# Performance work log

Measured on AMD Instinct MI355X. Metric: run time of the kernel, lower is better.

The kernel has to match this reference:

```python
import jax, jax.numpy as jnp
import numpy as np

DIM = 1024
HEADS = 16
HEAD_DIM = DIM // HEADS
MLP_HID = 4 * DIM
EPS = 1e-5


def layer_norm(x, g, b):
    mu = jnp.mean(x, axis=-1, keepdims=True)
    var = jnp.mean(jnp.square(x - mu), axis=-1, keepdims=True)
    return (x - mu) * jax.lax.rsqrt(var + EPS) * g + b


def setup_inputs() -> dict:
    key = jax.random.key(0)
    ks = jax.random.split(key, 8)
    s_in = 1.0 / np.sqrt(DIM)
    s_hid = 1.0 / np.sqrt(MLP_HID)
    return {
        "x": jax.random.normal(ks[0], (4, 2048, DIM), dtype=jnp.float32),
        "qkv_w": jax.random.uniform(ks[1], (3 * DIM, DIM), jnp.float32, -s_in, s_in),
        "proj_w": jax.random.uniform(ks[2], (DIM, DIM), jnp.float32, -s_in, s_in),
        "proj_b": jnp.zeros((DIM,), jnp.float32),
        "ln1_g": jnp.ones((DIM,), jnp.float32),
        "ln1_b": jnp.zeros((DIM,), jnp.float32),
        "w1": jax.random.uniform(ks[3], (MLP_HID, DIM), jnp.float32, -s_in, s_in),
        "b1": jnp.zeros((MLP_HID,), jnp.float32),
        "prelu_a": jnp.asarray(0.25, jnp.float32),
        "w2": jax.random.uniform(ks[4], (DIM, MLP_HID), jnp.float32, -s_hid, s_hid),
        "b2": jnp.zeros((DIM,), jnp.float32),
        "ln2_g": jnp.ones((DIM,), jnp.float32),
        "ln2_b": jnp.zeros((DIM,), jnp.float32),
    }


def reference(x, qkv_w, proj_w, proj_b, ln1_g, ln1_b, w1, b1, prelu_a, w2, b2, ln2_g, ln2_b):
    B, N, C = x.shape
    scale = HEAD_DIM ** (-0.5)

    # Multi-head self-attention (full NxN scores, softmax over keys)
    qkv = (x @ qkv_w.T).reshape(B, N, 3, HEADS, HEAD_DIM)
    qkv = jnp.transpose(qkv, (2, 0, 3, 1, 4))  # [3, B, H, N, hd]
    q, k, v = qkv[0] * scale, qkv[1], qkv[2]
    attn = jax.nn.softmax(jnp.einsum("bhnd,bhmd->bhnm", q, k), axis=-1)
    o = jnp.einsum("bhnm,bhmd->bhnd", attn, v)
    o = jnp.transpose(o, (0, 2, 1, 3)).reshape(B, N, C)
    o = o @ proj_w.T + proj_b

    # Post-norm residual 1
    x = layer_norm(x + o, ln1_g, ln1_b)

    # MLP: Linear -> (Dropout=identity in eval) -> PReLU -> Linear
    h = x @ w1.T + b1
    h = jnp.where(h >= 0, h, prelu_a * h)
    h = h @ w2.T + b2

    # Post-norm residual 2
    return layer_norm(x + h, ln2_g, ln2_b)
```

## Files before the change

kernel.cpp:

```cpp
#include <hip/hip_runtime.h>


typedef __attribute__((ext_vector_type(8))) short short8;
typedef __attribute__((ext_vector_type(4))) short short4v;
typedef __attribute__((ext_vector_type(4))) float floatx4;
typedef __attribute__((ext_vector_type(4))) int int4v;

__device__ __forceinline__ float bf2f(unsigned short u) {
    return __uint_as_float(((unsigned int)u) << 16);
}
__device__ __forceinline__ unsigned short f2bf(float f) {
    unsigned int u = __float_as_uint(f);
    u += 0x7FFFu + ((u >> 16) & 1u);
    return (unsigned short)(u >> 16);
}
__device__ __forceinline__ int pack2bf(float a, float b) {
    return (int)f2bf(a) | ((int)f2bf(b) << 16);
}
__device__ __forceinline__ unsigned int cvt_pk_bf16(float lo, float hi) {
    unsigned int r;
    asm("v_cvt_pk_bf16_f32 %0, %1, %2" : "=v"(r) : "v"(lo), "v"(hi));
    return r;
}

#define Q_PRESCALE 0.18033688011112043f

#if __has_builtin(__builtin_amdgcn_exp2f)
__device__ __forceinline__ float fast_exp2(float x) { return __builtin_amdgcn_exp2f(x); }
#else
__device__ __forceinline__ float fast_exp2(float x) { return __expf(x * 0.6931471805599453f); }
#endif

#if __has_builtin(__builtin_amdgcn_permlane32_swap) && __has_builtin(__builtin_amdgcn_permlane16_swap)
#define HAVE_PERMLANE 1
#else
#define HAVE_PERMLANE 0
#endif

__device__ __forceinline__ void async16(const unsigned short* g, unsigned short* l) {
    __builtin_amdgcn_global_load_lds(
        (const __attribute__((address_space(1))) unsigned int*)g,
        (__attribute__((address_space(3))) unsigned int*)l, 16, 0, 0);
}

__global__ __launch_bounds__(256)
void cvt_f2b(const float* __restrict__ in, unsigned short* __restrict__ out) {
    const int i = (blockIdx.x * 256 + threadIdx.x) * 4;
    float4 v = *(const float4*)&in[i];
    short4v o;
    o[0] = (short)f2bf(v.x); o[1] = (short)f2bf(v.y);
    o[2] = (short)f2bf(v.z); o[3] = (short)f2bf(v.w);
    *(short4v*)&out[i] = o;
}

__global__ __launch_bounds__(256)
void gemm_bt(const unsigned short* __restrict__ A,
             const unsigned short* __restrict__ W,
             const float* __restrict__ bias,
             const float* __restrict__ prelu,
             unsigned short* __restrict__ C,
             int N, int K, int qcols) {
    __shared__ alignas(16) unsigned short lA[128 * 64];
    __shared__ alignas(16) unsigned short lB[128 * 64];

    const int m0 = blockIdx.x * 128;
    const int n0 = blockIdx.y * 128;
    const int tid  = threadIdx.x;
    const int lane = tid & 63;
    const int wave = tid >> 6;
    const int wm = (wave >> 1) * 64;
    const int wn = (wave & 1) * 64;
    const int lr = lane & 15;
    const int lq = lane >> 4;

    floatx4 acc[4][4] = {};

    for (int k0 = 0; k0 < K; k0 += 64) {
        #pragma unroll
        for (int it = 0; it < 4; ++it) {
            const int i = it * 256 + tid;
            const int row = i >> 3;
            const int col = (i & 7) << 3;
            unsigned short* dstA = &lA[(it * 256 + wave * 64) * 8];
            unsigned short* dstB = &lB[(it * 256 + wave * 64) * 8];
            async16(&A[(size_t)(m0 + row) * K + k0 + col], dstA);
            async16(&W[(size_t)(n0 + row) * K + k0 + col], dstB);
        }
        __syncthreads();
        #pragma unroll
        for (int s = 0; s < 2; ++s) {
            short8 af[4], bfr[4];
            #pragma unroll
            for (int i = 0; i < 4; ++i)
                af[i] = *(const short8*)&lA[(wm + i * 16 + lr) * 64 + s * 32 + lq * 8];
            #pragma unroll
            for (int j = 0; j < 4; ++j)
                bfr[j] = *(const short8*)&lB[(wn + j * 16 + lr) * 64 + s * 32 + lq * 8];
            #pragma unroll
            for (int i = 0; i < 4; ++i)
                #pragma unroll
                for (int j = 0; j < 4; ++j)
                    acc[i][j] = __builtin_amdgcn_mfma_f32_16x16x32_bf16(
                        af[i], bfr[j], acc[i][j], 0, 0, 0);
        }
        __syncthreads();
    }

    const bool has_prelu = (prelu != nullptr);
    const float slope = has_prelu ? prelu[0] : 0.f;
    #pragma unroll
    for (int j = 0; j < 4; ++j) {
        int gc = n0 + wn + j * 16 + lr;
        float bv = bias ? bias[gc] : 0.f;
        const float cscale = (gc < qcols) ? Q_PRESCALE : 1.f;
        #pragma unroll
        for (int i = 0; i < 4; ++i) {
            int gr = m0 + wm + i * 16 + lq * 4;
            #pragma unroll
            for (int r = 0; r < 4; ++r) {
                float v = acc[i][j][r] + bv;
                if (has_prelu && v < 0.f) v *= slope;
                C[(size_t)(gr + r) * N + gc] = f2bf(v * cscale);
            }
        }
    }
}

__global__ __launch_bounds__(256)
void transpose_v(const unsigned short* __restrict__ qkv,
                 unsigned short* __restrict__ vt) {
    const int kt = blockIdx.x;
    const int bh = blockIdx.y;
    const int b = bh >> 4, h = bh & 15;
    __shared__ unsigned short tile[64 * 65];
    for (int t = threadIdx.x; t < 512; t += 256) {
        const int key = t >> 3, c8 = (t & 7) << 3;
        short8 v8 = *(const short8*)&qkv[((size_t)(b * 2048 + kt * 64 + key)) * 3072 +
                                         2048 + h * 64 + c8];
        #pragma unroll
        for (int e = 0; e < 8; ++e)
            tile[key * 65 + c8 + e] = (unsigned short)v8[e];
    }
    __syncthreads();
    for (int t = threadIdx.x; t < 512; t += 256) {
        const int d = t >> 3, k8 = (t & 7) << 3;
        short8 o;
        #pragma unroll
        for (int e = 0; e < 8; ++e)
            o[e] = (short)tile[(k8 + e) * 65 + d];
        *(short8*)&vt[((size_t)bh * 64 + d) * 2048 + kt * 64 + k8] = o;
    }
}

__global__ __launch_bounds__(256, 2)
void attn_kernel(const unsigned short* __restrict__ qkv,
                 const unsigned short* __restrict__ vt,
                 unsigned short* __restrict__ o_attn) {
    const int id = blockIdx.x;
    const int qg = id >> 6;
    const int bh = id & 63;
    const int b = bh >> 4, h = bh & 15;
    const int tid  = threadIdx.x;
    const int lane = tid & 63;
    const int wave = tid >> 6;
    const int lr = lane & 15;
    const int lq = lane >> 4;
    const int q0 = (qg * 4 + wave) * 64;
    const size_t row0 = (size_t)(b * 2048) * 3072;

    __shared__ alignas(16) unsigned short lK[2][64 * 64];
    __shared__ alignas(16) unsigned short lV[2][64 * 64];

    short8 qf[4][2];
    #pragma unroll
    for (int j = 0; j < 4; ++j)
        #pragma unroll
        for (int s = 0; s < 2; ++s)
            qf[j][s] = *(const short8*)&qkv[row0 + (size_t)(q0 + j * 16 + lr) * 3072 +
                                            h * 64 + s * 32 + lq * 8];

    floatx4 oacc[4][4] = {};
    float l_i[4] = {0.f, 0.f, 0.f, 0.f};

    const int srow = lane >> 3;
    const int scol = (((lane & 7) ^ srow)) << 3;
    const int kx = lr & 7;

    auto stage = [&](int bi, int kc) {
        #pragma unroll
        for (int it2 = 0; it2 < 2; ++it2) {
            const int it = wave * 2 + it2;
            const int row = it * 8 + srow;
            async16(&qkv[row0 + (size_t)(kc + row) * 3072 + 1024 + h * 64 + scol],
                    &lK[bi][it * 512 + lane * 8]);
            async16(&vt[((size_t)bh * 64 + row) * 2048 + kc + scol],
                    &lV[bi][it * 512 + lane * 8]);
        }
    };

    asm volatile("s_waitcnt vmcnt(0)" ::: "memory");
    stage(0, 0);

    #pragma unroll 1
    for (int c = 0; c < 32; ++c) {
        const int cur = c & 1;
        if (c + 1 < 32) {
            stage(cur ^ 1, (c + 1) * 64);
            asm volatile("s_waitcnt vmcnt(4)" ::: "memory");
        } else {
            asm volatile("s_waitcnt vmcnt(0)" ::: "memory");
        }
        __builtin_amdgcn_s_barrier();
        asm volatile("" ::: "memory");

        floatx4 sacc[4][4] = {};
        #pragma unroll
        for (int s = 0; s < 2; ++s) {
            short8 kf[4];
            #pragma unroll
            for (int i = 0; i < 4; ++i) {
                const int r = i * 16 + lr;
                kf[i] = *(const short8*)&lK[cur][r * 64 + (((s * 4 + lq) ^ kx) << 3)];
            }
            #pragma unroll
            for (int i = 0; i < 4; ++i)
                #pragma unroll
                for (int j = 0; j < 4; ++j)
                    sacc[i][j] = __builtin_amdgcn_mfma_f32_16x16x32_bf16(
                        kf[i], qf[j][s], sacc[i][j], 0, 0, 0);
        }

        unsigned int pkd[4][4][2];
        #pragma unroll
        for (int i = 0; i < 4; ++i)
            #pragma unroll
            for (int j = 0; j < 4; ++j) {
                const float e0 = fast_exp2(sacc[i][j][0]);
                const float e1 = fast_exp2(sacc[i][j][1]);
                const float e2 = fast_exp2(sacc[i][j][2]);
                const float e3 = fast_exp2(sacc[i][j][3]);
                l_i[j] += (e0 + e1) + (e2 + e3);
                pkd[i][j][0] = cvt_pk_bf16(e0, e1);
                pkd[i][j][1] = cvt_pk_bf16(e2, e3);
            }

        #pragma unroll
        for (int s = 0; s < 2; ++s) {
            short8 vf[4];
            #pragma unroll
            for (int i = 0; i < 4; ++i) {
                const int r = i * 16 + lr;
                vf[i] = *(const short8*)&lV[cur][r * 64 + (((s * 4 + lq) ^ kx) << 3)];
            }
            short8 bq[4];
            #pragma unroll
            for (int j = 0; j < 4; ++j) {
                int4v iv;
#if HAVE_PERMLANE
                auto p0 = __builtin_amdgcn_permlane32_swap(
                    pkd[2 * s][j][0], pkd[2 * s + 1][j][0], false, false);
                auto w0 = __builtin_amdgcn_permlane16_swap(p0[0], p0[1], false, false);
                auto p1 = __builtin_amdgcn_permlane32_swap(
                    pkd[2 * s][j][1], pkd[2 * s + 1][j][1], false, false);
                auto w1 = __builtin_amdgcn_permlane16_swap(p1[0], p1[1], false, false);
                iv[0] = (int)w0[0]; iv[1] = (int)w1[0];
                iv[2] = (int)w0[1]; iv[3] = (int)w1[1];
#else
                const int src0 = lr + ((lq & 1) * 2) * 16;
                const int src1 = src0 + 16;
                const bool hi = (lq >> 1) != 0;
                int a0 = __shfl((int)pkd[2 * s][j][0], src0, 64);
                int c0 = __shfl((int)pkd[2 * s + 1][j][0], src0, 64);
                int a1 = __shfl((int)pkd[2 * s][j][1], src0, 64);
                int c1 = __shfl((int)pkd[2 * s + 1][j][1], src0, 64);
                int a2 = __shfl((int)pkd[2 * s][j][0], src1, 64);
                int c2 = __shfl((int)pkd[2 * s + 1][j][0], src1, 64);
                int a3 = __shfl((int)pkd[2 * s][j][1], src1, 64);
                int c3 = __shfl((int)pkd[2 * s + 1][j][1], src1, 64);
                iv[0] = hi ? c0 : a0;
                iv[1] = hi ? c1 : a1;
                iv[2] = hi ? c2 : a2;
                iv[3] = hi ? c3 : a3;
#endif
                bq[j] = __builtin_bit_cast(short8, iv);
            }
            #pragma unroll
            for (int j = 0; j < 4; ++j)
                #pragma unroll
                for (int i = 0; i < 4; ++i)
                    oacc[i][j] = __builtin_amdgcn_mfma_f32_16x16x32_bf16(
                        vf[i], bq[j], oacc[i][j], 0, 0, 0);
        }

        asm volatile("s_waitcnt lgkmcnt(0)" ::: "memory");
        __builtin_amdgcn_s_barrier();
        asm volatile("" ::: "memory");
    }

    #pragma unroll
    for (int j = 0; j < 4; ++j) {
        l_i[j] += __shfl_xor(l_i[j], 16, 64);
        l_i[j] += __shfl_xor(l_i[j], 32, 64);
        const float rl = 1.f / l_i[j];
        const int q = q0 + j * 16 + lr;
        #pragma unroll
        for (int i = 0; i < 4; ++i) {
            int2 pk;
            pk.x = pack2bf(oacc[i][j][0] * rl, oacc[i][j][1] * rl);
            pk.y = pack2bf(oacc[i][j][2] * rl, oacc[i][j][3] * rl);
            *(int2*)&o_attn[((size_t)(b * 2048 + q)) * 1024 + h * 64 + i * 16 + lq * 4] = pk;
        }
    }
}

__global__ __launch_bounds__(256)
void ln_f32_bf16(const float* __restrict__ x,
                 const unsigned short* __restrict__ res,
                 const float* __restrict__ g,
                 const float* __restrict__ bta,
                 unsigned short* __restrict__ out) {
    const int row = blockIdx.x;
    const int t = threadIdx.x;
    const size_t base = (size_t)row * 1024;

    float4 xv = *(const float4*)&x[base + t * 4];
    short4v rv = *(const short4v*)&res[base + t * 4];
    float v[4] = { xv.x + bf2f((unsigned short)rv[0]),
                   xv.y + bf2f((unsigned short)rv[1]),
                   xv.z + bf2f((unsigned short)rv[2]),
                   xv.w + bf2f((unsigned short)rv[3]) };
    float s = 0.f, s2 = 0.f;
    #pragma unroll
    for (int k = 0; k < 4; ++k) { s += v[k]; s2 += v[k] * v[k]; }
    #pragma unroll
    for (int off = 32; off > 0; off >>= 1) {
        s  += __shfl_xor(s, off, 64);
        s2 += __shfl_xor(s2, off, 64);
    }
    __shared__ float red[8];
    const int wave = t >> 6;
    if ((t & 63) == 0) { red[wave] = s; red[4 + wave] = s2; }
    __syncthreads();
    s  = red[0] + red[1] + red[2] + red[3];
    s2 = red[4] + red[5] + red[6] + red[7];
    const float mean = s * (1.f / 1024.f);
    const float var  = fmaxf(s2 * (1.f / 1024.f) - mean * mean, 0.f);
    const float inv  = rsqrtf(var + 1e-5f);

    short4v ov;
    #pragma unroll
    for (int k = 0; k < 4; ++k) {
        int c = t * 4 + k;
        ov[k] = (short)f2bf((v[k] - mean) * inv * g[c] + bta[c]);
    }
    *(short4v*)&out[base + t * 4] = ov;
}

__global__ __launch_bounds__(256)
void ln_bf16_f32(const unsigned short* __restrict__ x,
                 const unsigned short* __restrict__ res,
                 const float* __restrict__ g,
                 const float* __restrict__ bta,
                 float* __restrict__ out) {
    const int row = blockIdx.x;
    const int t = threadIdx.x;
    const size_t base = (size_t)row * 1024;

    short4v xv = *(const short4v*)&x[base + t * 4];
    short4v rv = *(const short4v*)&res[base + t * 4];
    float v[4];
    float s = 0.f, s2 = 0.f;
    #pragma unroll
    for (int k = 0; k < 4; ++k) {
        v[k] = bf2f((unsigned short)xv[k]) + bf2f((unsigned short)rv[k]);
        s += v[k];
        s2 += v[k] * v[k];
    }
    #pragma unroll
    for (int off = 32; off > 0; off >>= 1) {
        s  += __shfl_xor(s, off, 64);
        s2 += __shfl_xor(s2, off, 64);
    }
    __shared__ float red[8];
    const int wave = t >> 6;
    if ((t & 63) == 0) { red[wave] = s; red[4 + wave] = s2; }
    __syncthreads();
    s  = red[0] + red[1] + red[2] + red[3];
    s2 = red[4] + red[5] + red[6] + red[7];
    const float mean = s * (1.f / 1024.f);
    const float var  = fmaxf(s2 * (1.f / 1024.f) - mean * mean, 0.f);
    const float inv  = rsqrtf(var + 1e-5f);

    float4 ov;
    ov.x = (v[0] - mean) * inv * g[t * 4 + 0] + bta[t * 4 + 0];
    ov.y = (v[1] - mean) * inv * g[t * 4 + 1] + bta[t * 4 + 1];
    ov.z = (v[2] - mean) * inv * g[t * 4 + 2] + bta[t * 4 + 2];
    ov.w = (v[3] - mean) * inv * g[t * 4 + 3] + bta[t * 4 + 3];
    *(float4*)&out[base + t * 4] = ov;
}

extern "C" void kernel_launch(void* const* d_in, const int* in_sizes, int n_in,
                              void* d_out, int out_size, void* d_ws, size_t ws_size,
                              hipStream_t stream) {
    const float* x      = (const float*)d_in[0];
    const float* qkv_w  = (const float*)d_in[1];
    const float* proj_w = (const float*)d_in[2];
    const float* proj_b = (const float*)d_in[3];
    const float* ln1_g  = (const float*)d_in[4];
    const float* ln1_b  = (const float*)d_in[5];
    const float* w1     = (const float*)d_in[6];
    const float* b1     = (const float*)d_in[7];
    const float* prelu  = (const float*)d_in[8];
    const float* w2     = (const float*)d_in[9];
    const float* b2     = (const float*)d_in[10];
    const float* ln2_g  = (const float*)d_in[11];
    const float* ln2_b  = (const float*)d_in[12];
    float* out = (float*)d_out;

    char* ws = (char*)d_ws;
    const size_t MB = 1024 * 1024;
    unsigned short* wqkvb  = (unsigned short*)(ws);
    unsigned short* wprojb = (unsigned short*)(ws + 6 * MB);
    unsigned short* w1b    = (unsigned short*)(ws + 8 * MB);
    unsigned short* w2b    = (unsigned short*)(ws + 16 * MB);
    unsigned short* xb     = (unsigned short*)(ws + 24 * MB);
    unsigned short* vtb    = (unsigned short*)(ws + 24 * MB);
    unsigned short* qkvb   = (unsigned short*)(ws + 40 * MB);
    unsigned short* oat    = (unsigned short*)(ws + 88 * MB);
    unsigned short* pout   = (unsigned short*)(ws + 24 * MB);
    unsigned short* x1b    = (unsigned short*)(ws + 40 * MB);
    unsigned short* h1     = (unsigned short*)(ws + 56 * MB);
    unsigned short* h2     = (unsigned short*)(ws + 24 * MB);

    cvt_f2b<<<8192, 256, 0, stream>>>(x,      xb);
    cvt_f2b<<<3072, 256, 0, stream>>>(qkv_w,  wqkvb);
    cvt_f2b<<<1024, 256, 0, stream>>>(proj_w, wprojb);
    cvt_f2b<<<4096, 256, 0, stream>>>(w1,     w1b);
    cvt_f2b<<<4096, 256, 0, stream>>>(w2,     w2b);

    gemm_bt<<<dim3(64, 24), 256, 0, stream>>>(xb, wqkvb, nullptr, nullptr,
                                              qkvb, 3072, 1024, 1024);
    transpose_v<<<dim3(32, 64), 256, 0, stream>>>(qkvb, vtb);
    attn_kernel<<<512, 256, 0, stream>>>(qkvb, vtb, oat);
    gemm_bt<<<dim3(64, 8), 256, 0, stream>>>(oat, wprojb, proj_b, nullptr,
                                             pout, 1024, 1024, 0);
    ln_f32_bf16<<<8192, 256, 0, stream>>>(x, pout, ln1_g, ln1_b, x1b);
    gemm_bt<<<dim3(64, 32), 256, 0, stream>>>(x1b, w1b, b1, prelu,
                                              h1, 4096, 1024, 0);
    gemm_bt<<<dim3(64, 8), 256, 0, stream>>>(h1, w2b, b2, nullptr,
                                             h2, 1024, 4096, 0);
    ln_bf16_f32<<<8192, 256, 0, stream>>>(x1b, h2, ln2_g, ln2_b, out);
}
```

Measured before the change: 567.5 us.

## Replace 128x128 GEMM with double-buffered 256x256 ping-pong MFMA kernel

Replaces the simple 128x128-tile bf16 GEMM with a 512-thread, 256x256-tile kernel. It double-buffers LDS and issues async global-to-LDS loads for the next K tiles while MFMAs run in four quadrant phases. It also XOR-swizzles LDS columns to avoid bank conflicts, remaps workgroup IDs across XCDs, and raises wave priority around the MFMA blocks. The aim is more data reuse per tile and overlap of loads with compute. The cost is a much larger LDS footprint and far fewer workgroups: only 128 for the proj and second MLP GEMMs, which may leave CUs idle.

```diff
diff --git a/kernel.cpp b/kernel.cpp
--- a/kernel.cpp
+++ b/kernel.cpp
@@ -53,77 +53,176 @@
     *(short4v*)&out[i] = o;
 }
 
-__global__ __launch_bounds__(256)
-void gemm_bt(const unsigned short* __restrict__ A,
+__global__ __launch_bounds__(512, 2)
+void gemm256(const unsigned short* __restrict__ A,
              const unsigned short* __restrict__ W,
              const float* __restrict__ bias,
              const float* __restrict__ prelu,
              unsigned short* __restrict__ C,
-             int N, int K, int qcols) {
-    __shared__ alignas(16) unsigned short lA[128 * 64];
-    __shared__ alignas(16) unsigned short lB[128 * 64];
-
-    const int m0 = blockIdx.x * 128;
-    const int n0 = blockIdx.y * 128;
+             int N, int K, int qcols, int NNT) {
+    __shared__ alignas(16) unsigned short lA[2][256 * 64];
+    __shared__ alignas(16) unsigned short lB[2][256 * 64];
+
+    const int nwg = gridDim.x;
+    const int orig = blockIdx.x;
+    const int q8 = nwg >> 3, r8 = nwg & 7, xx = orig & 7, rest = orig >> 3;
+    const int wgid = (xx < r8 ? xx * (q8 + 1) : r8 * (q8 + 1) + (xx - r8) * q8) + rest;
+    const int mt = wgid / NNT, nt = wgid % NNT;
+    const int m0 = mt * 256, n0 = nt * 256;
+
     const int tid  = threadIdx.x;
     const int lane = tid & 63;
     const int wave = tid >> 6;
-    const int wm = (wave >> 1) * 64;
-    const int wn = (wave & 1) * 64;
-    const int lr = lane & 15;
-    const int lq = lane >> 4;
-
-    floatx4 acc[4][4] = {};
-
-    for (int k0 = 0; k0 < K; k0 += 64) {
-        #pragma unroll
-        for (int it = 0; it < 4; ++it) {
-            const int i = it * 256 + tid;
-            const int row = i >> 3;
-            const int col = (i & 7) << 3;
-            unsigned short* dstA = &lA[(it * 256 + wave * 64) * 8];
-            unsigned short* dstB = &lB[(it * 256 + wave * 64) * 8];
-            async16(&A[(size_t)(m0 + row) * K + k0 + col], dstA);
-            async16(&W[(size_t)(n0 + row) * K + k0 + col], dstB);
-        }
-        __syncthreads();
-        #pragma unroll
-        for (int s = 0; s < 2; ++s) {
-            short8 af[4], bfr[4];
+    const int lr = lane & 15, lq = lane >> 4;
+    const int wrow = (wave >> 2) * 64;
+    const int wcol = (wave & 3) * 32;
+    const int srow = lane >> 3;
+    const int scol = ((lane & 7) * 8) ^ ((lane & 32) ? 16 : 0);
+    const int kxo  = (lq * 8) ^ ((lr & 4) ? 16 : 0);
+
+    const int NT = K >> 6;
+
+    floatx4 acc[2][2][4][2] = {};
+
+    auto stA = [&](int d, int tt, int h) {
+        #pragma unroll
+        for (int it = 0; it < 2; ++it) {
+            const int rb = h * 128 + (wave * 2 + it) * 8;
+            async16(&A[(size_t)(m0 + rb + srow) * K + tt * 64 + scol], &lA[d][rb * 64]);
+        }
+    };
+    auto stB = [&](int d, int tt, int h) {
+        #pragma unroll
+        for (int it = 0; it < 2; ++it) {
+            const int rb = h * 128 + (wave * 2 + it) * 8;
+            async16(&W[(size_t)(n0 + rb + srow) * K + tt * 64 + scol], &lB[d][rb * 64]);
+        }
+    };
+
+    stA(0, 0, 0); stB(0, 0, 0); stB(0, 0, 1); stA(0, 0, 1);
+    stA(1, 1, 0); stB(1, 1, 0); stB(1, 1, 1);
+    asm volatile("s_waitcnt vmcnt(6)" ::: "memory");
+    __builtin_amdgcn_s_barrier();
+    asm volatile("" ::: "memory");
+
+    short8 af[4][2], b0[2][2], b1[2][2];
+
+    for (int t = 0; t < NT; ++t) {
+        const int d = t & 1, e = d ^ 1;
+
+        #pragma unroll
+        for (int i = 0; i < 4; ++i)
+            #pragma unroll
+            for (int s = 0; s < 2; ++s)
+                af[i][s] = *(const short8*)&lA[d][(wrow + i * 16 + lr) * 64 + s * 32 + kxo];
+        #pragma unroll
+        for (int j = 0; j < 2; ++j)
+            #pragma unroll
+            for (int s = 0; s < 2; ++s)
+                b0[j][s] = *(const short8*)&lB[d][(wcol + j * 16 + lr) * 64 + s * 32 + kxo];
+        if (t + 1 < NT) stA(e, t + 1, 1);
+        __builtin_amdgcn_s_barrier();
+        asm volatile("s_waitcnt lgkmcnt(0)" ::: "memory");
+        __builtin_amdgcn_s_setprio(1);
+        #pragma unroll
+        for (int s = 0; s < 2; ++s)
             #pragma unroll
             for (int i = 0; i < 4; ++i)
-                af[i] = *(const short8*)&lA[(wm + i * 16 + lr) * 64 + s * 32 + lq * 8];
-            #pragma unroll
-            for (int j = 0; j < 4; ++j)
-                bfr[j] = *(const short8*)&lB[(wn + j * 16 + lr) * 64 + s * 32 + lq * 8];
+                #pragma unroll
+                for (int j = 0; j < 2; ++j)
+                    acc[0][0][i][j] = __builtin_amdgcn_mfma_f32_16x16x32_bf16(
+                        af[i][s], b0[j][s], acc[0][0][i][j], 0, 0, 0);
+        __builtin_amdgcn_s_setprio(0);
+        __builtin_amdgcn_s_barrier();
+        asm volatile("" ::: "memory");
+
+        #pragma unroll
+        for (int j = 0; j < 2; ++j)
+            #pragma unroll
+            for (int s = 0; s < 2; ++s)
+                b1[j][s] = *(const short8*)&lB[d][(128 + wcol + j * 16 + lr) * 64 + s * 32 + kxo];
+        if (t + 2 < NT) stA(d, t + 2, 0);
+        __builtin_amdgcn_s_barrier();
+        asm volatile("s_waitcnt lgkmcnt(0)" ::: "memory");
+        __builtin_amdgcn_s_setprio(1);
+        #pragma unroll
+        for (int s = 0; s < 2; ++s)
             #pragma unroll
             for (int i = 0; i < 4; ++i)
                 #pragma unroll
-                for (int j = 0; j < 4; ++j)
-                    acc[i][j] = __builtin_amdgcn_mfma_f32_16x16x32_bf16(
-                        af[i], bfr[j], acc[i][j], 0, 0, 0);
-        }
-        __syncthreads();
-    }
-
-    const bool has_prelu = (prelu != nullptr);
-    const float slope = has_prelu ? prelu[0] : 0.f;
-    #pragma unroll
-    for (int j = 0; j < 4; ++j) {
-        int gc = n0 + wn + j * 16 + lr;
-        float bv = bias ? bias[gc] : 0.f;
-        const float cscale = (gc < qcols) ? Q_PRESCALE : 1.f;
-        #pragma unroll
-        for (int i = 0; i < 4; ++i) {
-            int gr = m0 + wm + i * 16 + lq * 4;
-            #pragma unroll
-            for (int r = 0; r < 4; ++r) {
-                float v = acc[i][j][r] + bv;
-                if (has_prelu && v < 0.f) v *= slope;
-                C[(size_t)(gr + r) * N + gc] = f2bf(v * cscale);
+                for (int j = 0; j < 2; ++j)
+                    acc[0][1][i][j] = __builtin_amdgcn_mfma_f32_16x16x32_bf16(
+                        af[i][s], b1[j][s], acc[0][1][i][j], 0, 0, 0);
+        __builtin_amdgcn_s_setprio(0);
+        __builtin_amdgcn_s_barrier();
+        asm volatile("" ::: "memory");
+
+        #pragma unroll
+        for (int i = 0; i < 4; ++i)
+            #pragma unroll
+            for (int s = 0; s < 2; ++s)
+                af[i][s] = *(const short8*)&lA[d][(128 + wrow + i * 16 + lr) * 64 + s * 32 + kxo];
+        if (t + 2 < NT) stB(d, t + 2, 0);
+        __builtin_amdgcn_s_barrier();
+        asm volatile("s_waitcnt lgkmcnt(0)" ::: "memory");
+        __builtin_amdgcn_s_setprio(1);
+        #pragma unroll
+        for (int s = 0; s < 2; ++s)
+            #pragma unroll
+            for (int i = 0; i < 4; ++i)
+                #pragma unroll
+                for (int j = 0; j < 2; ++j)
+                    acc[1][1][i][j] = __builtin_amdgcn_mfma_f32_16x16x32_bf16(
+                        af[i][s], b1[j][s], acc[1][1][i][j], 0, 0, 0);
+        __builtin_amdgcn_s_setprio(0);
+        __builtin_amdgcn_s_barrier();
+        asm volatile("" ::: "memory");
+
+        if (t + 2 < NT) stB(d, t + 2, 1);
+        __builtin_amdgcn_s_barrier();
+        asm volatile("" ::: "memory");
+        __builtin_amdgcn_s_setprio(1);
+        #pragma unroll
+        for (int s = 0; s < 2; ++s)
+            #pragma unroll
+            for (int i = 0; i < 4; ++i)
+                #pragma unroll
+                for (int j = 0; j < 2; ++j)
+                    acc[1][0][i][j] = __builtin_amdgcn_mfma_f32_16x16x32_bf16(
+                        af[i][s], b0[j][s], acc[1][0][i][j], 0, 0, 0);
+        __builtin_amdgcn_s_setprio(0);
+        if (t + 2 < NT) {
+            asm volatile("s_waitcnt vmcnt(6)" ::: "memory");
+        } else {
+            asm volatile("s_waitcnt vmcnt(0)" ::: "memory");
+        }
+        __builtin_amdgcn_s_barrier();
+        asm volatile("" ::: "memory");
+    }
+
+    const bool hasb = (bias != nullptr);
+    const bool hasp = (prelu != nullptr);
+    const float slope = hasp ? prelu[0] : 0.f;
+    #pragma unroll
+    for (int mh = 0; mh < 2; ++mh)
+        #pragma unroll
+        for (int nh = 0; nh < 2; ++nh)
+            #pragma unroll
+            for (int j = 0; j < 2; ++j) {
+                const int gc = n0 + nh * 128 + wcol + j * 16 + lr;
+                const float bv = hasb ? bias[gc] : 0.f;
+                const float cs = (gc < qcols) ? Q_PRESCALE : 1.f;
+                #pragma unroll
+                for (int i = 0; i < 4; ++i) {
+                    const int gr = m0 + mh * 128 + wrow + i * 16 + lq * 4;
+                    #pragma unroll
+                    for (int r = 0; r < 4; ++r) {
+                        float v = acc[mh][nh][i][j][r] + bv;
+                        if (hasp && v < 0.f) v *= slope;
+                        C[(size_t)(gr + r) * N + gc] = f2bf(v * cs);
+                    }
+                }
             }
-        }
-    }
 }
 
 __global__ __launch_bounds__(256)
@@ -438,16 +537,16 @@
     cvt_f2b<<<4096, 256, 0, stream>>>(w1,     w1b);
     cvt_f2b<<<4096, 256, 0, stream>>>(w2,     w2b);
 
-    gemm_bt<<<dim3(64, 24), 256, 0, stream>>>(xb, wqkvb, nullptr, nullptr,
-                                              qkvb, 3072, 1024, 1024);
+    gemm256<<<dim3(32 * 12), 512, 0, stream>>>(xb, wqkvb, nullptr, nullptr,
+                                               qkvb, 3072, 1024, 1024, 12);
     transpose_v<<<dim3(32, 64), 256, 0, stream>>>(qkvb, vtb);
     attn_kernel<<<512, 256, 0, stream>>>(qkvb, vtb, oat);
-    gemm_bt<<<dim3(64, 8), 256, 0, stream>>>(oat, wprojb, proj_b, nullptr,
-                                             pout, 1024, 1024, 0);
+    gemm256<<<dim3(32 * 4), 512, 0, stream>>>(oat, wprojb, proj_b, nullptr,
+                                              pout, 1024, 1024, 0, 4);
     ln_f32_bf16<<<8192, 256, 0, stream>>>(x, pout, ln1_g, ln1_b, x1b);
-    gemm_bt<<<dim3(64, 32), 256, 0, stream>>>(x1b, w1b, b1, prelu,
-                                              h1, 4096, 1024, 0);
-    gemm_bt<<<dim3(64, 8), 256, 0, stream>>>(h1, w2b, b2, nullptr,
-                                             h2, 1024, 4096, 0);
+    gemm256<<<dim3(32 * 16), 512, 0, stream>>>(x1b, w1b, b1, prelu,
+                                               h1, 4096, 1024, 0, 16);
+    gemm256<<<dim3(32 * 4), 512, 0, stream>>>(h1, w2b, b2, nullptr,
+                                              h2, 1024, 4096, 0, 4);
     ln_bf16_f32<<<8192, 256, 0, stream>>>(x1b, h2, ln2_g, ln2_b, out);
 }
```

Result: no change. 567.9 us (+0.1%).
